# Performance work log

Measured on AMD Instinct MI355X. Metric: run time of the kernel, lower is better.

## Reference

```python
import jax, jax.numpy as jnp
import numpy as np

H = 16        # num_attention_heads
KV = 4        # num_key_value_heads
DH = 128      # head_dim
THETA = 10000.0
MIN_VAL = -1000000000000000.0


def _rope_tables(L):
    # inv_freq: (DH/2,), positions: (L,)
    inv_freq = 1.0 / (THETA ** (jnp.arange(0, DH, 2, dtype=jnp.float32) / DH))
    pos = jnp.arange(L, dtype=jnp.float32)
    freq = pos[:, None] * inv_freq[None, :]          # (L, DH/2)
    emb = jnp.concatenate([freq, freq], axis=-1)      # (L, DH)
    return jnp.cos(emb), jnp.sin(emb)


def _apply_rope(x, cos, sin):
    # x: (B, h, L, DH); cos/sin: (L, DH)
    left = x[..., : DH // 2]
    right = -x[..., DH // 2 :]
    rot = jnp.concatenate([right, left], axis=-1)
    return x * cos[None, None] + rot * sin[None, None]


def setup_inputs() -> dict:
    key = jax.random.key(0)
    ks = jax.random.split(key, 5)
    B, L, D = 2, 2048, 2048
    s = 0.02
    return {
        "hidden_state": jax.random.normal(ks[0], (B, L, D), jnp.float32),
        "attention_mask": jnp.ones((B, L), jnp.int32),
        "Wq": jax.random.normal(ks[1], (H * DH, D), jnp.float32) * s,
        "Wk": jax.random.normal(ks[2], (KV * DH, D), jnp.float32) * s,
        "Wv": jax.random.normal(ks[3], (KV * DH, D), jnp.float32) * s,
        "Wo": jax.random.normal(ks[4], (D, D), jnp.float32) * s,
    }


def reference(hidden_state, attention_mask, Wq, Wk, Wv, Wo):
    B, L, D = hidden_state.shape
    cos, sin = _rope_tables(L)

    q = jnp.einsum('bld,ed->ble', hidden_state, Wq).reshape(B, L, H, DH).transpose(0, 2, 1, 3)
    k = jnp.einsum('bld,ed->ble', hidden_state, Wk).reshape(B, L, KV, DH).transpose(0, 2, 1, 3)
    v = jnp.einsum('bld,ed->ble', hidden_state, Wv).reshape(B, L, KV, DH).transpose(0, 2, 1, 3)

    q = _apply_rope(q, cos, sin)
    k = _apply_rope(k, cos, sin)

    # GQA: repeat each KV head H/KV times -> (B, H, L, DH)
    g = H // KV
    k = jnp.repeat(k, g, axis=1)
    v = jnp.repeat(v, g, axis=1)

    scores = jnp.einsum('bhqd,bhkd->bhqk', q, k) / np.sqrt(DH)  # (B,H,L,L)

    causal = jnp.triu(jnp.full((L, L), MIN_VAL, jnp.float32), k=1)[None, None]  # (1,1,L,L)
    pad = (attention_mask == 0)[:, None, None, :]  # (B,1,1,L)
    mask = jnp.where(pad, MIN_VAL, causal)
    scores = scores + mask

    attn = jax.nn.softmax(scores.astype(jnp.float32), axis=-1).astype(q.dtype)
    out = jnp.einsum('bhqk,bhkd->bhqd', attn, v)
    out = out.transpose(0, 2, 1, 3).reshape(B, L, H * DH)
    return jnp.einsum('ble,de->bld', out, Wo)
```

## Files before the change

kernel.cpp:

```cpp
#include <hip/hip_runtime.h>
#include <cstdint>
#include <cmath>


typedef __bf16 bf16_t;
typedef __bf16 bf16x8 __attribute__((ext_vector_type(8)));
typedef __bf16 bf16x4 __attribute__((ext_vector_type(4)));
typedef float  f32x4  __attribute__((ext_vector_type(4)));

#define HQ   16
#define HKV  4
#define GQA  4
#define DHD  128
#define BB   2
#define LL   2048
#define DDIM 2048
#define MINV (-1e15f)

static __device__ __forceinline__ f32x4 mfma16(bf16x8 a, bf16x8 b, f32x4 c) {
  return __builtin_amdgcn_mfma_f32_16x16x32_bf16(a, b, c, 0, 0, 0);
}

static __device__ __forceinline__ void gld16(const bf16_t* g, bf16_t* l) {
  __builtin_amdgcn_global_load_lds(
      (const __attribute__((address_space(1))) void*)g,
      (__attribute__((address_space(3))) void*)l,
      16, 0, 0);
}

struct CastArgs {
  const float* s[5];
  bf16_t* d[5];
  int n[5];
};

__global__ __launch_bounds__(256) void cast5_kernel(CastArgs a) {
  const int t = blockIdx.y;
  const int i8 = (blockIdx.x * 256 + threadIdx.x) * 8;
  if (i8 >= a.n[t]) return;
  const float4* s = (const float4*)(a.s[t] + i8);
  float4 x = s[0], y = s[1];
  bf16x8 o = {(bf16_t)x.x, (bf16_t)x.y, (bf16_t)x.z, (bf16_t)x.w,
              (bf16_t)y.x, (bf16_t)y.y, (bf16_t)y.z, (bf16_t)y.w};
  *(bf16x8*)(a.d[t] + i8) = o;
}

template <int STORE>
__global__ __launch_bounds__(256) void gemm_tile(const bf16_t* __restrict__ A,
                                                 const bf16_t* __restrict__ W,
                                                 void* __restrict__ C0,
                                                 bf16_t* __restrict__ Ck,
                                                 bf16_t* __restrict__ Cv,
                                                 int M, int N, int K) {
  __shared__ __align__(16) bf16_t As[128 * 32];
  __shared__ __align__(16) bf16_t Bs[128 * 32];
  const int tid  = threadIdx.x;
  const int lane = tid & 63;
  const int wave = tid >> 6;
  const int l15  = lane & 15;
  const int quad = lane >> 4;
  const int m0 = blockIdx.y * 128;
  const int n0 = blockIdx.x * 128;

  const int srow = wave * 32 + (lane >> 2);
  const int scol = (lane & 3) * 8;
  const bf16_t* ag = A + (size_t)(m0 + srow) * K + scol;
  const bf16_t* wg = W + (size_t)(n0 + srow) * K + scol;
  bf16_t* al = As + wave * 1024;
  bf16_t* bl = Bs + wave * 1024;

  const int wm = (wave >> 1) * 64;
  const int wn = (wave & 1) * 64;

  f32x4 acc[4][4];
#pragma unroll
  for (int mi = 0; mi < 4; mi++)
#pragma unroll
    for (int ni = 0; ni < 4; ni++) acc[mi][ni] = {0.f, 0.f, 0.f, 0.f};

  for (int k0 = 0; k0 < K; k0 += 32) {
    __syncthreads();
    gld16(ag + k0, al);
    gld16(ag + k0 + (size_t)16 * K, al + 512);
    gld16(wg + k0, bl);
    gld16(wg + k0 + (size_t)16 * K, bl + 512);
    __syncthreads();
    bf16x8 af[4], bfr[4];
#pragma unroll
    for (int mi = 0; mi < 4; mi++)
      af[mi] = *(const bf16x8*)(As + (wm + mi * 16 + l15) * 32 + quad * 8);
#pragma unroll
    for (int ni = 0; ni < 4; ni++)
      bfr[ni] = *(const bf16x8*)(Bs + (wn + ni * 16 + l15) * 32 + quad * 8);
#pragma unroll
    for (int mi = 0; mi < 4; mi++)
#pragma unroll
      for (int ni = 0; ni < 4; ni++)
        acc[mi][ni] = mfma16(af[mi], bfr[ni], acc[mi][ni]);
  }

  if (STORE == 2) {
    float* C = (float*)C0;
#pragma unroll
    for (int mi = 0; mi < 4; mi++) {
      const int row = m0 + wm + mi * 16 + quad * 4;
#pragma unroll
      for (int ni = 0; ni < 4; ni++) {
        const int col = n0 + wn + ni * 16 + l15;
#pragma unroll
        for (int i = 0; i < 4; i++)
          C[(size_t)(row + i) * N + col] = acc[mi][ni][i];
      }
    }
  } else {
    if (n0 < 2048) {
      bf16_t* C = (bf16_t*)C0;
#pragma unroll
      for (int mi = 0; mi < 4; mi++) {
        const int row = m0 + wm + mi * 16 + quad * 4;
#pragma unroll
        for (int ni = 0; ni < 4; ni++) {
          const int col = n0 + wn + ni * 16 + l15;
#pragma unroll
          for (int i = 0; i < 4; i++)
            C[(size_t)(row + i) * 2048 + col] = (bf16_t)acc[mi][ni][i];
        }
      }
    } else if (n0 < 2560) {
#pragma unroll
      for (int mi = 0; mi < 4; mi++) {
        const int row = m0 + wm + mi * 16 + quad * 4;
#pragma unroll
        for (int ni = 0; ni < 4; ni++) {
          const int col = n0 - 2048 + wn + ni * 16 + l15;
#pragma unroll
          for (int i = 0; i < 4; i++)
            Ck[(size_t)(row + i) * 512 + col] = (bf16_t)acc[mi][ni][i];
        }
      }
    } else {
#pragma unroll
      for (int mi = 0; mi < 4; mi++) {
        const int row = m0 + wm + mi * 16 + quad * 4;
        const int b = row >> 11;
        const int l0 = row & (LL - 1);
#pragma unroll
        for (int ni = 0; ni < 4; ni++) {
          const int kvcol = n0 - 2560 + wn + ni * 16 + l15;
          const int kvh = kvcol >> 7, d = kvcol & 127;
          bf16x4 w4 = {(bf16_t)acc[mi][ni][0], (bf16_t)acc[mi][ni][1],
                       (bf16_t)acc[mi][ni][2], (bf16_t)acc[mi][ni][3]};
          *(bf16x4*)(Cv + ((size_t)(b * HKV + kvh) * DHD + d) * LL + l0) = w4;
        }
      }
    }
  }
}

__global__ void rope_kernel(bf16_t* __restrict__ q, bf16_t* __restrict__ k,
                            const int* __restrict__ amask, float* __restrict__ bias) {
  const int nq = BB * LL * HQ * 64;
  const int nk = BB * LL * HKV * 64;
  int id = blockIdx.x * blockDim.x + threadIdx.x;
  if (id >= nq + nk) {
    int id2 = id - (nq + nk);
    if (id2 < BB * LL) bias[id2] = (amask[id2] == 0) ? MINV : 0.0f;
    return;
  }
  bf16_t* base;
  int heads, idx;
  if (id < nq) { base = q; heads = HQ; idx = id; }
  else         { base = k; heads = HKV; idx = id - nq; }
  int d = idx & 63; idx >>= 6;
  int hh = idx % heads;
  int bl = idx / heads;
  int l = bl & (LL - 1);
  bf16_t* p = base + ((size_t)bl * heads + hh) * DHD + d;
  float x1 = (float)p[0];
  float x2 = (float)p[64];
  float invf = __expf(-(float)d * 0.14391156862532788f);
  float fr = (float)l * invf;
  float s, c;
  __sincosf(fr, &s, &c);
  p[0]  = (bf16_t)(x1 * c - x2 * s);
  p[64] = (bf16_t)(x2 * c + x1 * s);
}

#define KSTR 136
#define VSTR 72

__global__ __launch_bounds__(256, 2) void flash_attn2(const bf16_t* __restrict__ q,
                                                      const bf16_t* __restrict__ k,
                                                      const bf16_t* __restrict__ vt,
                                                      const float* __restrict__ bias,
                                                      bf16_t* __restrict__ o) {
  __shared__ __align__(16) bf16_t Kbuf[64 * KSTR];
  __shared__ __align__(16) bf16_t Vbuf[128 * VSTR];
  __shared__ __align__(16) bf16_t Pbuf[4 * 2 * 1024];

  const int tid  = threadIdx.x;
  const int lane = tid & 63;
  const int wave = tid >> 6;
  const int l15  = lane & 15;
  const int quad = lane >> 4;

  const int c  = blockIdx.x >> 5;
  const int bh = blockIdx.x & 31;
  const int b  = bh >> 4;
  const int h  = bh & 15;
  const int kv = h >> 2;

  const int q0[2] = { c * 64 + wave * 16, (31 - c) * 64 + wave * 16 };
  const int nrounds = 32 - c;
  const float kScale = 0.08838834764831845f;

  bf16x8 qf[2][4];
#pragma unroll
  for (int qt = 0; qt < 2; qt++) {
    const bf16_t* qb = q + ((size_t)(b * LL + q0[qt] + l15)) * (HQ * DHD) + h * DHD + quad * 8;
#pragma unroll
    for (int t = 0; t < 4; t++) qf[qt][t] = *(const bf16x8*)(qb + 32 * t);
  }

  f32x4 acc[8][2];
#pragma unroll
  for (int mt = 0; mt < 8; mt++)
#pragma unroll
    for (int qt = 0; qt < 2; qt++) acc[mt][qt] = {0.f, 0.f, 0.f, 0.f};
  float m_i[2] = {-1e30f, -1e30f};
  float l_i[2] = {0.f, 0.f};

  const bf16_t* kg_base = k + ((size_t)(b * LL)) * (HKV * DHD) + kv * DHD;
  const bf16_t* vg_base = vt + ((size_t)(b * HKV + kv) * DHD) * LL;
  const float*  bias_b  = bias + b * LL;

  const int krow = tid >> 4, kch = tid & 15;
  const int vrow = tid >> 3, vch = tid & 7;

  for (int r = 0; r < nrounds; r++) {
    const int j0 = r * 64;
    {
      const bf16_t* kg = kg_base + (size_t)(j0 + krow) * (HKV * DHD) + kch * 8;
      const bf16_t* vg = vg_base + (size_t)vrow * LL + j0 + vch * 8;
      bf16x8 kl[4], vl[4];
#pragma unroll
      for (int p = 0; p < 4; p++) kl[p] = *(const bf16x8*)(kg + (size_t)p * 16 * (HKV * DHD));
#pragma unroll
      for (int p = 0; p < 4; p++) vl[p] = *(const bf16x8*)(vg + (size_t)p * 32 * LL);
      __syncthreads();
#pragma unroll
      for (int p = 0; p < 4; p++) *(bf16x8*)(Kbuf + (krow + p * 16) * KSTR + kch * 8) = kl[p];
#pragma unroll
      for (int p = 0; p < 4; p++) *(bf16x8*)(Vbuf + (vrow + p * 32) * VSTR + vch * 8) = vl[p];
      __syncthreads();
    }
    const bool act_a = (r <= c);

    f32x4 s[2][4];
#pragma unroll
    for (int kt = 0; kt < 4; kt++) {
      const bf16_t* kr = Kbuf + (kt * 16 + l15) * KSTR + quad * 8;
      f32x4 s0 = {0.f, 0.f, 0.f, 0.f};
      f32x4 s1 = {0.f, 0.f, 0.f, 0.f};
#pragma unroll
      for (int t = 0; t < 4; t++) {
        bf16x8 kf = *(const bf16x8*)(kr + t * 32);
        if (act_a) s0 = mfma16(kf, qf[0][t], s0);
        s1 = mfma16(kf, qf[1][t], s1);
      }
      s[0][kt] = s0; s[1][kt] = s1;
    }

    f32x4 bv[4];
#pragma unroll
    for (int kt = 0; kt < 4; kt++) bv[kt] = *(const f32x4*)(bias_b + j0 + kt * 16 + quad * 4);

    bf16x8 pf[2][2];
#pragma unroll
    for (int qt = 0; qt < 2; qt++) {
      if (qt == 0 && !act_a) continue;
      const int qrow = q0[qt] + l15;
      const bool diag = (j0 + 63 > q0[qt]);
      float mx = -1e30f;
#pragma unroll
      for (int kt = 0; kt < 4; kt++) {
        f32x4 sv = s[qt][kt];
#pragma unroll
        for (int i = 0; i < 4; i++) {
          float x = sv[i] + bv[kt][i];
          if (diag) {
            int key = j0 + kt * 16 + quad * 4 + i;
            if (key > qrow) x = MINV;
          }
          sv[i] = x;
          mx = fmaxf(mx, x);
        }
        s[qt][kt] = sv;
      }
      mx = fmaxf(mx, __shfl_xor(mx, 16));
      mx = fmaxf(mx, __shfl_xor(mx, 32));
      const float mn = fmaxf(m_i[qt], mx);
      const float alpha = __expf((m_i[qt] - mn) * kScale);
      m_i[qt] = mn;
      float sum = 0.f;
      bf16_t* pw = Pbuf + wave * 2048 + qt * 1024 + l15 * 8 + (quad & 1) * 4;
#pragma unroll
      for (int kt = 0; kt < 4; kt++) {
        f32x4 sv = s[qt][kt];
        bf16x4 p4;
#pragma unroll
        for (int i = 0; i < 4; i++) {
          float p = __expf((sv[i] - mn) * kScale);
          sum += p;
          p4[i] = (bf16_t)p;
        }
        *(bf16x4*)(pw + (kt >> 1) * 512 + ((kt & 1) * 2 + (quad >> 1)) * 128) = p4;
      }
      sum += __shfl_xor(sum, 16);
      sum += __shfl_xor(sum, 32);
      l_i[qt] = l_i[qt] * alpha + sum;
#pragma unroll
      for (int mt = 0; mt < 8; mt++) {
        acc[mt][qt][0] *= alpha; acc[mt][qt][1] *= alpha;
        acc[mt][qt][2] *= alpha; acc[mt][qt][3] *= alpha;
      }
      const bf16_t* pr = Pbuf + wave * 2048 + qt * 1024 + lane * 8;
      pf[qt][0] = *(const bf16x8*)(pr);
      pf[qt][1] = *(const bf16x8*)(pr + 512);
    }

#pragma unroll
    for (int mt = 0; mt < 8; mt++) {
      const bf16_t* vr = Vbuf + (mt * 16 + l15) * VSTR + quad * 8;
      bf16x8 vf0 = *(const bf16x8*)(vr);
      bf16x8 vf1 = *(const bf16x8*)(vr + 32);
      if (act_a) {
        acc[mt][0] = mfma16(vf0, pf[0][0], acc[mt][0]);
        acc[mt][0] = mfma16(vf1, pf[0][1], acc[mt][0]);
      }
      acc[mt][1] = mfma16(vf0, pf[1][0], acc[mt][1]);
      acc[mt][1] = mfma16(vf1, pf[1][1], acc[mt][1]);
    }
  }

#pragma unroll
  for (int qt = 0; qt < 2; qt++) {
    const float invl = 1.0f / l_i[qt];
    bf16_t* ob = o + ((size_t)(b * LL + q0[qt] + l15)) * (HQ * DHD) + h * DHD + quad * 4;
#pragma unroll
    for (int mt = 0; mt < 8; mt++) {
      f32x4 a = acc[mt][qt];
      bf16x4 w = {(bf16_t)(a[0] * invl), (bf16_t)(a[1] * invl),
                  (bf16_t)(a[2] * invl), (bf16_t)(a[3] * invl)};
      *(bf16x4*)(ob + mt * 16) = w;
    }
  }
}

extern "C" void kernel_launch(void* const* d_in, const int* in_sizes, int n_in,
                              void* d_out, int out_size, void* d_ws, size_t ws_size,
                              hipStream_t stream) {
  const float* hidden = (const float*)d_in[0];
  const int*   amask  = (const int*)d_in[1];
  const float* Wq     = (const float*)d_in[2];
  const float* Wk     = (const float*)d_in[3];
  const float* Wv     = (const float*)d_in[4];
  const float* Wo     = (const float*)d_in[5];
  float* out = (float*)d_out;

  const int M = BB * LL;
  const size_t MB = 1u << 20;
  char* ws = (char*)d_ws;
  bf16_t* hid_b   = (bf16_t*)(ws);
  bf16_t* q_ws    = (bf16_t*)(ws + 16 * MB);
  bf16_t* attn_ws = (bf16_t*)(ws + 32 * MB);
  bf16_t* k_ws    = (bf16_t*)(ws + 48 * MB);
  bf16_t* vt_ws   = (bf16_t*)(ws + 52 * MB);
  bf16_t* wqkv_b  = (bf16_t*)(ws + 56 * MB);
  bf16_t* wq_b    = wqkv_b;
  bf16_t* wk_b    = (bf16_t*)(ws + 64 * MB);
  bf16_t* wv_b    = (bf16_t*)(ws + 66 * MB);
  bf16_t* wo_b    = (bf16_t*)(ws + 68 * MB);
  float*  bias_ws = (float*)(ws);

  CastArgs ca;
  ca.s[0] = hidden; ca.d[0] = hid_b; ca.n[0] = BB * LL * DDIM;
  ca.s[1] = Wq;     ca.d[1] = wq_b;  ca.n[1] = HQ * DHD * DDIM;
  ca.s[2] = Wk;     ca.d[2] = wk_b;  ca.n[2] = HKV * DHD * DDIM;
  ca.s[3] = Wv;     ca.d[3] = wv_b;  ca.n[3] = HKV * DHD * DDIM;
  ca.s[4] = Wo;     ca.d[4] = wo_b;  ca.n[4] = DDIM * DDIM;
  {
    int maxn = BB * LL * DDIM;
    dim3 g((maxn / 8 + 255) / 256, 5);
    cast5_kernel<<<g, 256, 0, stream>>>(ca);
  }

  gemm_tile<3><<<dim3(3072 / 128, M / 128), 256, 0, stream>>>(
      hid_b, wqkv_b, q_ws, k_ws, vt_ws, M, 3072, DDIM);

  {
    int total = BB * LL * (HQ + HKV) * 64 + BB * LL;
    rope_kernel<<<(total + 255) / 256, 256, 0, stream>>>(q_ws, k_ws, amask, bias_ws);
  }

  flash_attn2<<<BB * HQ * 16, 256, 0, stream>>>(q_ws, k_ws, vt_ws, bias_ws, attn_ws);

  gemm_tile<2><<<dim3(DDIM / 128, M / 128), 256, 0, stream>>>(
      attn_ws, wo_b, (void*)out, nullptr, nullptr, M, DDIM, DDIM);
}
```

Baseline: 319.7 us.

## Keep softmax probabilities in registers and swizzle K/V shared-memory layouts

The attention kernel no longer round-trips P through shared memory. It feeds the probability registers directly into 16x16x16 bf16 MFMAs, with V stored in an XOR-swizzled, permuted layout so its fragments line up. The softmax scale and log2e are folded into Q during RoPE so exp2 can be used directly. Rescaling is skipped when the running max grows by less than a threshold, and block ordering is remapped. The cost is twice as many smaller MFMAs for PV, plus a precision risk if the lazy-rescale threshold is set wrong.

```diff
diff --git a/kernel.cpp b/kernel.cpp
--- a/kernel.cpp
+++ b/kernel.cpp
@@ -16,10 +16,33 @@
 #define LL   2048
 #define DDIM 2048
 #define MINV (-1e15f)
+#define QSC  0.12751744f
 
 static __device__ __forceinline__ f32x4 mfma16(bf16x8 a, bf16x8 b, f32x4 c) {
   return __builtin_amdgcn_mfma_f32_16x16x32_bf16(a, b, c, 0, 0, 0);
 }
+
+static __device__ __forceinline__ f32x4 mfma16k16(bf16x4 a, bf16x4 b, f32x4 c) {
+#if __has_builtin(__builtin_amdgcn_mfma_f32_16x16x16bf16_1k)
+  typedef short s4 __attribute__((ext_vector_type(4)));
+  union U { bf16x4 h; s4 s; };
+  U ua, ub; ua.h = a; ub.h = b;
+  return __builtin_amdgcn_mfma_f32_16x16x16bf16_1k(ua.s, ub.s, c, 0, 0, 0);
+#elif __has_builtin(__builtin_amdgcn_mfma_f32_16x16x16_bf16)
+  return __builtin_amdgcn_mfma_f32_16x16x16_bf16(a, b, c, 0, 0, 0);
+#else
+  f32x4 d;
+  asm volatile("v_mfma_f32_16x16x16_bf16 %0, %1, %2, %3"
+               : "=v"(d) : "v"(a), "v"(b), "v"(c));
+  return d;
+#endif
+}
+
+#if __has_builtin(__builtin_amdgcn_exp2f)
+#define EXP2F(x) __builtin_amdgcn_exp2f(x)
+#else
+#define EXP2F(x) exp2f(x)
+#endif
 
 static __device__ __forceinline__ void gld16(const bf16_t* g, bf16_t* l) {
   __builtin_amdgcn_global_load_lds(
@@ -169,8 +192,9 @@
   }
   bf16_t* base;
   int heads, idx;
-  if (id < nq) { base = q; heads = HQ; idx = id; }
-  else         { base = k; heads = HKV; idx = id - nq; }
+  float sc;
+  if (id < nq) { base = q; heads = HQ; idx = id; sc = QSC; }
+  else         { base = k; heads = HKV; idx = id - nq; sc = 1.0f; }
   int d = idx & 63; idx >>= 6;
   int hh = idx % heads;
   int bl = idx / heads;
@@ -182,21 +206,17 @@
   float fr = (float)l * invf;
   float s, c;
   __sincosf(fr, &s, &c);
-  p[0]  = (bf16_t)(x1 * c - x2 * s);
-  p[64] = (bf16_t)(x2 * c + x1 * s);
-}
-
-#define KSTR 136
-#define VSTR 72
+  p[0]  = (bf16_t)((x1 * c - x2 * s) * sc);
+  p[64] = (bf16_t)((x2 * c + x1 * s) * sc);
+}
 
 __global__ __launch_bounds__(256, 2) void flash_attn2(const bf16_t* __restrict__ q,
                                                       const bf16_t* __restrict__ k,
                                                       const bf16_t* __restrict__ vt,
                                                       const float* __restrict__ bias,
                                                       bf16_t* __restrict__ o) {
-  __shared__ __align__(16) bf16_t Kbuf[64 * KSTR];
-  __shared__ __align__(16) bf16_t Vbuf[128 * VSTR];
-  __shared__ __align__(16) bf16_t Pbuf[4 * 2 * 1024];
+  __shared__ __align__(16) bf16_t Kbuf[64 * 128];
+  __shared__ __align__(16) bf16_t Vbuf[128 * 64];
 
   const int tid  = threadIdx.x;
   const int lane = tid & 63;
@@ -204,15 +224,18 @@
   const int l15  = lane & 15;
   const int quad = lane >> 4;
 
-  const int c  = blockIdx.x >> 5;
-  const int bh = blockIdx.x & 31;
+  const int bi   = blockIdx.x;
+  const int half = bi >> 8;
+  const int jj   = bi & 255;
+  const int cc   = jj >> 5;
+  const int c    = half ? (15 - cc) : cc;
+  const int bh = jj & 31;
   const int b  = bh >> 4;
   const int h  = bh & 15;
   const int kv = h >> 2;
 
   const int q0[2] = { c * 64 + wave * 16, (31 - c) * 64 + wave * 16 };
   const int nrounds = 32 - c;
-  const float kScale = 0.08838834764831845f;
 
   bf16x8 qf[2][4];
 #pragma unroll
@@ -236,6 +259,11 @@
 
   const int krow = tid >> 4, kch = tid & 15;
   const int vrow = tid >> 3, vch = tid & 7;
+  const int vc0  = ((vch >> 2) << 5) + (((vch << 1) & 3) << 3) + (((vch >> 1) & 1) << 2);
+  const int vblo = vc0 * 2;
+  const int ksw  = (krow & 7) << 4;
+  const int vsw  = (vrow & 7) << 4;
+  const int rsw  = (l15 & 7) << 4;
 
   for (int r = 0; r < nrounds; r++) {
     const int j0 = r * 64;
@@ -249,9 +277,16 @@
       for (int p = 0; p < 4; p++) vl[p] = *(const bf16x8*)(vg + (size_t)p * 32 * LL);
       __syncthreads();
 #pragma unroll
-      for (int p = 0; p < 4; p++) *(bf16x8*)(Kbuf + (krow + p * 16) * KSTR + kch * 8) = kl[p];
-#pragma unroll
-      for (int p = 0; p < 4; p++) *(bf16x8*)(Vbuf + (vrow + p * 32) * VSTR + vch * 8) = vl[p];
+      for (int p = 0; p < 4; p++)
+        *(bf16x8*)((char*)Kbuf + (size_t)(krow + p * 16) * 256 + ((kch * 16) ^ ksw)) = kl[p];
+#pragma unroll
+      for (int p = 0; p < 4; p++) {
+        char* vbase = (char*)Vbuf + (size_t)(vrow + p * 32) * 128;
+        bf16x4 lo4 = __builtin_shufflevector(vl[p], vl[p], 0, 1, 2, 3);
+        bf16x4 hi4 = __builtin_shufflevector(vl[p], vl[p], 4, 5, 6, 7);
+        *(bf16x4*)(vbase + (vblo ^ vsw)) = lo4;
+        *(bf16x4*)(vbase + ((vblo + 16) ^ vsw)) = hi4;
+      }
       __syncthreads();
     }
     const bool act_a = (r <= c);
@@ -259,12 +294,12 @@
     f32x4 s[2][4];
 #pragma unroll
     for (int kt = 0; kt < 4; kt++) {
-      const bf16_t* kr = Kbuf + (kt * 16 + l15) * KSTR + quad * 8;
+      const char* kr = (const char*)Kbuf + (size_t)(kt * 16 + l15) * 256;
       f32x4 s0 = {0.f, 0.f, 0.f, 0.f};
       f32x4 s1 = {0.f, 0.f, 0.f, 0.f};
 #pragma unroll
       for (int t = 0; t < 4; t++) {
-        bf16x8 kf = *(const bf16x8*)(kr + t * 32);
+        bf16x8 kf = *(const bf16x8*)(kr + ((quad * 16 + t * 64) ^ rsw));
         if (act_a) s0 = mfma16(kf, qf[0][t], s0);
         s1 = mfma16(kf, qf[1][t], s1);
       }
@@ -275,7 +310,7 @@
 #pragma unroll
     for (int kt = 0; kt < 4; kt++) bv[kt] = *(const f32x4*)(bias_b + j0 + kt * 16 + quad * 4);
 
-    bf16x8 pf[2][2];
+    bf16x4 pf[2][4];
 #pragma unroll
     for (int qt = 0; qt < 2; qt++) {
       if (qt == 0 && !act_a) continue;
@@ -299,47 +334,55 @@
       }
       mx = fmaxf(mx, __shfl_xor(mx, 16));
       mx = fmaxf(mx, __shfl_xor(mx, 32));
-      const float mn = fmaxf(m_i[qt], mx);
-      const float alpha = __expf((m_i[qt] - mn) * kScale);
-      m_i[qt] = mn;
+      if (!__all(mx <= m_i[qt] + 8.0f)) {
+        const float mn = fmaxf(m_i[qt], mx);
+        const float alpha = EXP2F(m_i[qt] - mn);
+        m_i[qt] = mn;
+        l_i[qt] *= alpha;
+#pragma unroll
+        for (int mt = 0; mt < 8; mt++) {
+          acc[mt][qt][0] *= alpha; acc[mt][qt][1] *= alpha;
+          acc[mt][qt][2] *= alpha; acc[mt][qt][3] *= alpha;
+        }
+      }
+      const float mn = m_i[qt];
       float sum = 0.f;
-      bf16_t* pw = Pbuf + wave * 2048 + qt * 1024 + l15 * 8 + (quad & 1) * 4;
 #pragma unroll
       for (int kt = 0; kt < 4; kt++) {
         f32x4 sv = s[qt][kt];
         bf16x4 p4;
 #pragma unroll
         for (int i = 0; i < 4; i++) {
-          float p = __expf((sv[i] - mn) * kScale);
+          float p = EXP2F(sv[i] - mn);
           sum += p;
           p4[i] = (bf16_t)p;
         }
-        *(bf16x4*)(pw + (kt >> 1) * 512 + ((kt & 1) * 2 + (quad >> 1)) * 128) = p4;
+        pf[qt][kt] = p4;
       }
       sum += __shfl_xor(sum, 16);
       sum += __shfl_xor(sum, 32);
-      l_i[qt] = l_i[qt] * alpha + sum;
-#pragma unroll
-      for (int mt = 0; mt < 8; mt++) {
-        acc[mt][qt][0] *= alpha; acc[mt][qt][1] *= alpha;
-        acc[mt][qt][2] *= alpha; acc[mt][qt][3] *= alpha;
-      }
-      const bf16_t* pr = Pbuf + wave * 2048 + qt * 1024 + lane * 8;
-      pf[qt][0] = *(const bf16x8*)(pr);
-      pf[qt][1] = *(const bf16x8*)(pr + 512);
+      l_i[qt] += sum;
     }
 
 #pragma unroll
     for (int mt = 0; mt < 8; mt++) {
-      const bf16_t* vr = Vbuf + (mt * 16 + l15) * VSTR + quad * 8;
-      bf16x8 vf0 = *(const bf16x8*)(vr);
-      bf16x8 vf1 = *(const bf16x8*)(vr + 32);
+      const char* vr = (const char*)Vbuf + (size_t)(mt * 16 + l15) * 128;
+      bf16x8 v01 = *(const bf16x8*)(vr + ((quad * 16) ^ rsw));
+      bf16x8 v23 = *(const bf16x8*)(vr + ((64 + quad * 16) ^ rsw));
+      bf16x4 va = __builtin_shufflevector(v01, v01, 0, 1, 2, 3);
+      bf16x4 vb = __builtin_shufflevector(v01, v01, 4, 5, 6, 7);
+      bf16x4 vc = __builtin_shufflevector(v23, v23, 0, 1, 2, 3);
+      bf16x4 vd = __builtin_shufflevector(v23, v23, 4, 5, 6, 7);
       if (act_a) {
-        acc[mt][0] = mfma16(vf0, pf[0][0], acc[mt][0]);
-        acc[mt][0] = mfma16(vf1, pf[0][1], acc[mt][0]);
-      }
-      acc[mt][1] = mfma16(vf0, pf[1][0], acc[mt][1]);
-      acc[mt][1] = mfma16(vf1, pf[1][1], acc[mt][1]);
+        acc[mt][0] = mfma16k16(va, pf[0][0], acc[mt][0]);
+        acc[mt][0] = mfma16k16(vb, pf[0][1], acc[mt][0]);
+        acc[mt][0] = mfma16k16(vc, pf[0][2], acc[mt][0]);
+        acc[mt][0] = mfma16k16(vd, pf[0][3], acc[mt][0]);
+      }
+      acc[mt][1] = mfma16k16(va, pf[1][0], acc[mt][1]);
+      acc[mt][1] = mfma16k16(vb, pf[1][1], acc[mt][1]);
+      acc[mt][1] = mfma16k16(vc, pf[1][2], acc[mt][1]);
+      acc[mt][1] = mfma16k16(vd, pf[1][3], acc[mt][1]);
     }
   }
 
```

Measured after the change: 344.0 us. 1.08x slower.
